# Performance work log

Measured on AMD Instinct MI355X. Metric: run time of the kernel, lower is better.

Reference implementation:

```python
import jax, jax.numpy as jnp
import numpy as np
from jax import lax

B, IMG, P, C_IN, E, H, NAX = 128, 224, 16, 1, 96, 4, 14
N = NAX * NAX  # 196 patches


def _ln(x, g, b, axes=(-1,)):
    mu = jnp.mean(x, axes, keepdims=True)
    v = jnp.var(x, axes, keepdims=True)
    return (x - mu) * lax.rsqrt(v + 1e-5) * g + b


def _embed3d(p):
    # p: [B, N, E]. Torch code rotates pair (2i,2i+1) by theta_i*col (row loop)
    # then theta_i*row (col loop) in-place => total angle theta_i*(row+col).
    bsz = p.shape[0]
    f = p.transpose(0, 2, 1).reshape(bsz, E, NAX, NAX)
    i = jnp.arange(E // 2, dtype=jnp.float32)
    theta = 10000.0 ** (-2.0 * i / E)  # [48]
    pos = jnp.arange(NAX, dtype=jnp.float32)
    ang = theta[:, None, None] * (pos[None, :, None] + pos[None, None, :])  # [48,14,14]
    cos, sin = jnp.cos(ang), jnp.sin(ang)
    xe, ye = f[:, 0::2], f[:, 1::2]  # [B,48,14,14] each
    rx = xe * cos - ye * sin
    ry = xe * sin + ye * cos
    f = jnp.stack([rx, ry], axis=2).reshape(bsz, E, NAX, NAX)  # re-interleave pairs
    return f.reshape(bsz, E, N).transpose(0, 2, 1)


def _mhsa(x, g, bt, Wqkv, bqkv, Wo, bo):
    # standard pre-norm residual MHSA block (MHSelfAttentionBlock assumed)
    h = _ln(x, g, bt)
    qkv = h @ Wqkv + bqkv  # [B,N,3E]
    q, k, v = jnp.split(qkv, 3, axis=-1)
    d = E // H
    def heads(t):
        return t.reshape(t.shape[0], N, H, d).transpose(0, 2, 1, 3)  # [B,H,N,d]
    q, k, v = heads(q), heads(k), heads(v)
    s = jnp.einsum('bhqd,bhkd->bhqk', q, k) / jnp.sqrt(jnp.float32(d))
    a = jax.nn.softmax(s, axis=-1)
    o = jnp.einsum('bhqk,bhkd->bhqd', a, v).transpose(0, 2, 1, 3).reshape(x.shape[0], N, E)
    return x + o @ Wo + bo


def _convT(x, w, b):
    # torch ConvTranspose2d(k=4, s=2, p=1); w: [C_in, C_out, 4, 4]
    wt = jnp.transpose(jnp.flip(w, (2, 3)), (1, 0, 2, 3))  # OIHW, flipped
    y = lax.conv_general_dilated(x, wt, (1, 1), ((2, 2), (2, 2)), lhs_dilation=(2, 2),
                                 dimension_numbers=('NCHW', 'OIHW', 'NCHW'))
    return y + b[None, :, None, None]


def _forward(x, timestep, Wp, bp, Wt1, bt1, Wt2, bt2,
             a0_g, a0_b, a0_Wqkv, a0_bqkv, a0_Wo, a0_bo,
             a1_g, a1_b, a1_Wqkv, a1_bqkv, a1_Wo, a1_bo,
             Wm0, bm0, Wm1, bm1, Wm2, bm2,
             Wd1, bd1, l1g, l1b, Wd2, bd2, l2g, l2b, Wd3, bd3, l3g, l3b, Wd4, bd4):
    # timestep embedding: emb = -log(0.5)*t -> [sin, cos] -> MLP
    e = 0.6931471805599453 * timestep[0]
    tv = jnp.stack([jnp.sin(e), jnp.cos(e)])  # [2]
    time = jax.nn.silu(tv @ Wt1 + bt1) @ Wt2 + bt2  # [E]
    # patch embed: conv stride 16
    p = lax.conv_general_dilated(x, Wp, (P, P), 'VALID',
                                 dimension_numbers=('NCHW', 'OIHW', 'NCHW'))
    p = (p + bp[None, :, None, None]).reshape(x.shape[0], E, N).transpose(0, 2, 1)  # [B,N,E]
    p = _embed3d(p)
    p = _mhsa(p, a0_g, a0_b, a0_Wqkv, a0_bqkv, a0_Wo, a0_bo)
    p = _mhsa(p, a1_g, a1_b, a1_Wqkv, a1_bqkv, a1_Wo, a1_bo)
    p = p + time
    p = jax.nn.silu(p @ Wm0 + bm0)
    p = jax.nn.silu(p @ Wm1 + bm1)
    p = jax.nn.silu(p @ Wm2 + bm2)
    # unpatchify decoder
    f = p.transpose(0, 2, 1).reshape(x.shape[0], E, NAX, NAX)
    f = jax.nn.silu(_ln(_convT(f, Wd1, bd1), l1g, l1b, (-2, -1)))  # [B,48,28,28]
    f = jax.nn.silu(_ln(_convT(f, Wd2, bd2), l2g, l2b, (-2, -1)))  # [B,24,56,56]
    f = jax.nn.silu(_ln(_convT(f, Wd3, bd3), l3g, l3b, (-2, -1)))  # [B,12,112,112]
    f = jax.nn.silu(_convT(f, Wd4, bd4))                            # [B,1,224,224]
    return jnp.clip(f, 0.0, 1.0)


def setup_inputs() -> dict:
    ks = jax.random.split(jax.random.key(0), 40)
    rn = lambda k, s: (jax.random.normal(k, s, jnp.float32) * 0.02)
    inp = {
        'x': jax.random.normal(ks[0], (B, C_IN, IMG, IMG), jnp.float32),
        'timestep': jax.random.uniform(ks[1], (1,), jnp.float32),
        'Wp': rn(ks[2], (E, C_IN, P, P)), 'bp': jnp.zeros((E,), jnp.float32),
        'Wt1': rn(ks[3], (2, 128)), 'bt1': jnp.zeros((128,), jnp.float32),
        'Wt2': rn(ks[4], (128, E)), 'bt2': jnp.zeros((E,), jnp.float32),
        'a0_g': jnp.ones((E,), jnp.float32), 'a0_b': jnp.zeros((E,), jnp.float32),
        'a0_Wqkv': rn(ks[5], (E, 3 * E)), 'a0_bqkv': jnp.zeros((3 * E,), jnp.float32),
        'a0_Wo': rn(ks[6], (E, E)), 'a0_bo': jnp.zeros((E,), jnp.float32),
        'a1_g': jnp.ones((E,), jnp.float32), 'a1_b': jnp.zeros((E,), jnp.float32),
        'a1_Wqkv': rn(ks[7], (E, 3 * E)), 'a1_bqkv': jnp.zeros((3 * E,), jnp.float32),
        'a1_Wo': rn(ks[8], (E, E)), 'a1_bo': jnp.zeros((E,), jnp.float32),
        'Wm0': rn(ks[9], (E, E)), 'bm0': jnp.zeros((E,), jnp.float32),
        'Wm1': rn(ks[10], (E, E)), 'bm1': jnp.zeros((E,), jnp.float32),
        'Wm2': rn(ks[11], (E, E)), 'bm2': jnp.zeros((E,), jnp.float32),
        'Wd1': rn(ks[12], (E, 48, 4, 4)), 'bd1': jnp.zeros((48,), jnp.float32),
        'l1g': jnp.ones((28, 28), jnp.float32), 'l1b': jnp.zeros((28, 28), jnp.float32),
        'Wd2': rn(ks[13], (48, 24, 4, 4)), 'bd2': jnp.zeros((24,), jnp.float32),
        'l2g': jnp.ones((56, 56), jnp.float32), 'l2b': jnp.zeros((56, 56), jnp.float32),
        'Wd3': rn(ks[14], (24, 12, 4, 4)), 'bd3': jnp.zeros((12,), jnp.float32),
        'l3g': jnp.ones((112, 112), jnp.float32), 'l3b': jnp.zeros((112, 112), jnp.float32),
        'Wd4': rn(ks[15], (12, 1, 4, 4)), 'bd4': jnp.zeros((1,), jnp.float32),
    }
    return inp


def reference(x, timestep, Wp, bp, Wt1, bt1, Wt2, bt2,
              a0_g, a0_b, a0_Wqkv, a0_bqkv, a0_Wo, a0_bo,
              a1_g, a1_b, a1_Wqkv, a1_bqkv, a1_Wo, a1_bo,
              Wm0, bm0, Wm1, bm1, Wm2, bm2,
              Wd1, bd1, l1g, l1b, Wd2, bd2, l2g, l2b, Wd3, bd3, l3g, l3b, Wd4, bd4):
    return _forward(x, timestep, Wp, bp, Wt1, bt1, Wt2, bt2,
                    a0_g, a0_b, a0_Wqkv, a0_bqkv, a0_Wo, a0_bo,
                    a1_g, a1_b, a1_Wqkv, a1_bqkv, a1_Wo, a1_bo,
                    Wm0, bm0, Wm1, bm1, Wm2, bm2,
                    Wd1, bd1, l1g, l1b, Wd2, bd2, l2g, l2b, Wd3, bd3, l3g, l3b, Wd4, bd4)
```

## Files before the change

kernel.cpp:

```cpp
#include <hip/hip_runtime.h>
#include <cmath>


#define B_   128
#define NPATCH 196
#define M_ROWS (B_*NPATCH)
#define E_   96

typedef _Float16 half8 __attribute__((ext_vector_type(8)));
typedef _Float16 half4v __attribute__((ext_vector_type(4)));
typedef float f32x4 __attribute__((ext_vector_type(4)));

__global__ void k_time(const float* __restrict__ ts,
                       const float* __restrict__ Wt1, const float* __restrict__ bt1,
                       const float* __restrict__ Wt2, const float* __restrict__ bt2,
                       float* __restrict__ timev)
{
    __shared__ float h[128];
    float e = 0.69314718055994530942f * ts[0];
    float sv = sinf(e), cv = cosf(e);
    int t = threadIdx.x;
    float z = sv * Wt1[t] + cv * Wt1[128 + t] + bt1[t];
    h[t] = z / (1.f + expf(-z));
    __syncthreads();
    if (t < 96) {
        float acc = bt2[t];
        for (int j = 0; j < 128; ++j) acc += h[j] * Wt2[j * 96 + t];
        timev[t] = acc;
    }
}

__global__ void __launch_bounds__(256) k_zstat(float* __restrict__ stat)
{
    int i = blockIdx.x * 256 + threadIdx.x;
    if (i < 21504) stat[i] = 0.f;
}

__global__ void __launch_bounds__(256) k_repack(const float* __restrict__ w1,
                                                const float* __restrict__ w2,
                                                const float* __restrict__ w3,
                                                const float* __restrict__ w4f,
                                                float* __restrict__ wr)
{
    int i = blockIdx.x * 256 + threadIdx.x;
    const float* src; int CIN, COUT, e; float* dst;
    if      (i < 73728) { src = w1;  CIN = 96; COUT = 48; e = i;          dst = wr; }
    else if (i < 92160) { src = w2;  CIN = 48; COUT = 24; e = i - 73728;  dst = wr + 73728; }
    else if (i < 96768) { src = w3;  CIN = 24; COUT = 12; e = i - 92160;  dst = wr + 92160; }
    else if (i < 96960) { src = w4f; CIN = 12; COUT = 1;  e = i - 96768;  dst = wr + 96768; }
    else return;
    int per = CIN * COUT * 4;
    int par = e / per, rem = e % per;
    int ci = rem / (COUT * 4);
    int o  = (rem >> 2) % COUT;
    int j  = rem & 3;
    int ry = par >> 1, rx = par & 1;
    int wy = (j < 2)  ? (3 - ry) : (1 - ry);
    int wx = (j & 1)  ? (1 - rx) : (3 - rx);
    dst[e] = src[(ci * COUT + o) * 16 + wy * 4 + wx];
}

__global__ void __launch_bounds__(256) k_wcvtc(const float* __restrict__ w1,
                                               _Float16* __restrict__ wc)
{
    int i = blockIdx.x * 256 + threadIdx.x;
    if (i >= 4 * 48 * 384) return;
    int p = i / 18432, rem = i % 18432;
    int o = rem / 384, k = rem % 384;
    int tap = k / 96, ci = k % 96;
    int ry = p >> 1, rx = p & 1;
    int wy = (tap < 2) ? (3 - ry) : (1 - ry);
    int wx = (tap & 1) ? (1 - rx) : (3 - rx);
    wc[i] = (_Float16)w1[(ci * 48 + o) * 16 + wy * 4 + wx];
}

__global__ void __launch_bounds__(256) k_wcvt2(const float* __restrict__ w2,
                                               _Float16* __restrict__ wc2)
{
    int i = blockIdx.x * 256 + threadIdx.x;
    if (i >= 4 * 32 * 192) return;
    int p = i / 6144, rem = i % 6144;
    int o = rem / 192, k = rem % 192;
    int tap = k / 48, ci = k % 48;
    int ry = p >> 1, rx = p & 1;
    int wy = (tap < 2) ? (3 - ry) : (1 - ry);
    int wx = (tap & 1) ? (1 - rx) : (3 - rx);
    wc2[i] = (o < 24) ? (_Float16)w2[(ci * 24 + o) * 16 + wy * 4 + wx]
                      : (_Float16)0.f;
}

__global__ void __launch_bounds__(256) k_wcvt3(const float* __restrict__ w3,
                                               _Float16* __restrict__ wc3)
{
    int i = blockIdx.x * 256 + threadIdx.x;
    if (i >= 4 * 16 * 96) return;
    int p = i / 1536, rem = i % 1536;
    int o = rem / 96, k = rem % 96;
    int tap = k / 24, ci = k % 24;
    int ry = p >> 1, rx = p & 1;
    int wy = (tap < 2) ? (3 - ry) : (1 - ry);
    int wx = (tap & 1) ? (1 - rx) : (3 - rx);
    wc3[i] = (o < 12) ? (_Float16)w3[(ci * 12 + o) * 16 + wy * 4 + wx]
                      : (_Float16)0.f;
}

__global__ void __launch_bounds__(256) k_wcvt(const float* __restrict__ qkv0,
                                              const float* __restrict__ qkv1,
                                              const float* __restrict__ wo0,
                                              const float* __restrict__ wo1,
                                              const float* __restrict__ wm0,
                                              const float* __restrict__ wm1,
                                              const float* __restrict__ wm2,
                                              _Float16* __restrict__ wh)
{
    int i = blockIdx.x * 256 + threadIdx.x;
    const float* src; int N; int e;
    if      (i < 27648)  { src = qkv0; N = 288; e = i; }
    else if (i < 55296)  { src = qkv1; N = 288; e = i - 27648; }
    else if (i < 64512)  { src = wo0;  N = 96;  e = i - 55296; }
    else if (i < 73728)  { src = wo1;  N = 96;  e = i - 64512; }
    else if (i < 82944)  { src = wm0;  N = 96;  e = i - 73728; }
    else if (i < 92160)  { src = wm1;  N = 96;  e = i - 82944; }
    else if (i < 101376) { src = wm2;  N = 96;  e = i - 92160; }
    else return;
    int n = e / 96, k = e % 96;
    wh[i] = (_Float16)src[k * N + n];
}

__global__ void __launch_bounds__(256) k_zb_h(_Float16* __restrict__ xinh)
{
    int i = blockIdx.x * 256 + threadIdx.x;
    if (i >= 128 * 60 * 96) return;
    int b = i / 5760, r = i % 5760;
    int pos = r / 96, ch = r % 96;
    int py, px;
    if      (pos < 16) { py = 0;        px = pos; }
    else if (pos < 32) { py = 15;       px = pos - 16; }
    else if (pos < 46) { py = pos - 31; px = 0; }
    else               { py = pos - 45; px = 15; }
    xinh[((size_t)(b * 256) + py * 16 + px) * 96 + ch] = (_Float16)0.f;
}

__global__ void __launch_bounds__(256) k_patch_mfma(const float* __restrict__ x,
                                                    const float* __restrict__ Wp,
                                                    const float* __restrict__ bp,
                                                    float* __restrict__ out)
{
    __shared__ __align__(16) _Float16 Ah[64 * 136];
    __shared__ __align__(16) _Float16 Wh[96 * 136];
    int t = threadIdx.x;
    int p0 = blockIdx.x * 64;
    int wave = t >> 6, lane = t & 63;
    int lm = lane & 15, quad = lane >> 4;
    f32x4 acc[6];
    #pragma unroll
    for (int nt = 0; nt < 6; ++nt) acc[nt] = (f32x4){0.f, 0.f, 0.f, 0.f};

    for (int kc = 0; kc < 2; ++kc) {
        __syncthreads();
        for (int i = t; i < 512; i += 256) {
            int lp = i >> 3, pyl = i & 7;
            int patch = p0 + lp;
            int b = patch / NPATCH, n = patch % NPATCH;
            int ny = n / 14, nx = n % 14;
            const float4* s4 = (const float4*)(x +
                ((size_t)(b * 224) + ny * 16 + kc * 8 + pyl) * 224 + nx * 16);
            float4 v0 = s4[0], v1 = s4[1], v2 = s4[2], v3 = s4[3];
            half8 h0, h1;
            h0[0]=(_Float16)v0.x; h0[1]=(_Float16)v0.y; h0[2]=(_Float16)v0.z; h0[3]=(_Float16)v0.w;
            h0[4]=(_Float16)v1.x; h0[5]=(_Float16)v1.y; h0[6]=(_Float16)v1.z; h0[7]=(_Float16)v1.w;
            h1[0]=(_Float16)v2.x; h1[1]=(_Float16)v2.y; h1[2]=(_Float16)v2.z; h1[3]=(_Float16)v2.w;
            h1[4]=(_Float16)v3.x; h1[5]=(_Float16)v3.y; h1[6]=(_Float16)v3.z; h1[7]=(_Float16)v3.w;
            *(half8*)&Ah[lp * 136 + pyl * 16]     = h0;
            *(half8*)&Ah[lp * 136 + pyl * 16 + 8] = h1;
        }
        for (int i = t; i < 1536; i += 256) {
            int e = i >> 4, s = i & 15;
            const float4* s4 = (const float4*)(Wp + e * 256 + kc * 128 + s * 8);
            float4 v0 = s4[0], v1 = s4[1];
            half8 h0;
            h0[0]=(_Float16)v0.x; h0[1]=(_Float16)v0.y; h0[2]=(_Float16)v0.z; h0[3]=(_Float16)v0.w;
            h0[4]=(_Float16)v1.x; h0[5]=(_Float16)v1.y; h0[6]=(_Float16)v1.z; h0[7]=(_Float16)v1.w;
            *(half8*)&Wh[e * 136 + s * 8] = h0;
        }
        __syncthreads();
        half8 af[4];
        #pragma unroll
        for (int ks = 0; ks < 4; ++ks)
            af[ks] = *(const half8*)&Ah[(wave * 16 + lm) * 136 + ks * 32 + quad * 8];
        #pragma unroll
        for (int ks = 0; ks < 4; ++ks) {
            #pragma unroll
            for (int nt = 0; nt < 6; ++nt) {
                half8 bf = *(const half8*)&Wh[(nt * 16 + lm) * 136 + ks * 32 + quad * 8];
                acc[nt] = __builtin_amdgcn_mfma_f32_16x16x32_f16(af[ks], bf, acc[nt], 0, 0, 0);
            }
        }
    }

    #pragma unroll
    for (int nt = 0; nt < 6; ++nt) {
        #pragma unroll
        for (int r = 0; r < 4; ++r) {
            int e = nt * 16 + lm;
            int lp = wave * 16 + quad * 4 + r;
            int patch = p0 + lp;
            int n = patch % NPATCH;
            int ny = n / 14, nx = n % 14;
            float yx = (float)(ny + nx);
            float v = acc[nt][r] + bp[e];
            float other = __shfl_xor(v, 1);
            float fi = (float)(e >> 1);
            float theta = expf(fi * (-2.f / 96.f) * 9.210340371976184f);
            float ang = theta * yx;
            float c = cosf(ang), s = sinf(ang);
            float outv = (lm & 1) ? (other * s + v * c) : (v * c - other * s);
            out[(size_t)patch * 96 + e] = outv;
        }
    }
}

__global__ void __launch_bounds__(256) k_ln_row(const float* __restrict__ x,
                                                const float* __restrict__ g,
                                                const float* __restrict__ bv,
                                                _Float16* __restrict__ out, int M)
{
    int lane = threadIdx.x & 63;
    int gw = (blockIdx.x * 256 + threadIdx.x) >> 6;
    int nw = (gridDim.x * 256) >> 6;
    float g0 = g[lane], b0 = bv[lane];
    float g1 = 0.f, b1 = 0.f;
    if (lane < 32) { g1 = g[64 + lane]; b1 = bv[64 + lane]; }
    for (int r = gw; r < M; r += nw) {
        const float* xr = x + (size_t)r * 96;
        float a = xr[lane];
        float c = (lane < 32) ? xr[64 + lane] : 0.f;
        float s = a + c, q = a * a + c * c;
        #pragma unroll
        for (int off = 32; off; off >>= 1) {
            s += __shfl_xor(s, off);
            q += __shfl_xor(q, off);
        }
        float mu = s * (1.f / 96.f);
        float rstd = rsqrtf(q * (1.f / 96.f) - mu * mu + 1e-5f);
        _Float16* orow = out + (size_t)r * 96;
        orow[lane] = (_Float16)((a - mu) * rstd * g0 + b0);
        if (lane < 32) orow[64 + lane] = (_Float16)((c - mu) * rstd * g1 + b1);
    }
}

template<int NCHUNKS, int OUTMODE, bool SILU, bool RES, bool ADDTIME, bool AHALF>
__global__ void __launch_bounds__(256) k_gemm_mfma(const void* __restrict__ A,
                                                   const _Float16* __restrict__ Wt,
                                                   const float* __restrict__ bias,
                                                   const float* __restrict__ res,
                                                   const float* __restrict__ timev,
                                                   void* __restrict__ outp)
{
    __shared__ __align__(16) _Float16 Ah[64 * 96];
    __shared__ __align__(16) _Float16 Wh[96 * 96];
    constexpr int NTOT = NCHUNKS * 96;
    int t = threadIdx.x;
    size_t row0 = (size_t)blockIdx.x * 64;

    if constexpr (AHALF) {
        const uint4* a4 = (const uint4*)((const _Float16*)A + row0 * 96);
        uint4* dst = (uint4*)Ah;
        for (int i = t; i < 768; i += 256) dst[i] = a4[i];
    } else {
        const float4* a4 = (const float4*)((const float*)A + row0 * 96);
        for (int i = t; i < 1536; i += 256) {
            float4 v = a4[i];
            half4v hv;
            hv[0] = (_Float16)v.x; hv[1] = (_Float16)v.y;
            hv[2] = (_Float16)v.z; hv[3] = (_Float16)v.w;
            *(half4v*)&Ah[i * 4] = hv;
        }
    }

    int wave = t >> 6, lane = t & 63;
    int lm = lane & 15, quad = lane >> 4;
    const f32x4 vzero = {0.f, 0.f, 0.f, 0.f};

    for (int ch = blockIdx.y; ch < NCHUNKS; ch += gridDim.y) {
        __syncthreads();
        {
            const uint4* src = (const uint4*)(Wt + (size_t)ch * 9216);
            uint4* dst = (uint4*)Wh;
            for (int i = t; i < 1152; i += 256) dst[i] = src[i];
        }
        __syncthreads();

        half8 af[3];
        #pragma unroll
        for (int ks = 0; ks < 3; ++ks)
            af[ks] = *(const half8*)&Ah[(wave * 16 + lm) * 96 + ks * 32 + quad * 8];

        f32x4 acc[6];
        #pragma unroll
        for (int ct = 0; ct < 6; ++ct) acc[ct] = vzero;

        #pragma unroll
        for (int ct = 0; ct < 6; ++ct) {
            #pragma unroll
            for (int ks = 0; ks < 3; ++ks) {
                half8 bf = *(const half8*)&Wh[(ct * 16 + lm) * 96 + ks * 32 + quad * 8];
                acc[ct] = __builtin_amdgcn_mfma_f32_16x16x32_f16(af[ks], bf, acc[ct], 0, 0, 0);
            }
        }

        #pragma unroll
        for (int ct = 0; ct < 6; ++ct) {
            #pragma unroll
            for (int r = 0; r < 4; ++r) {
                int lr = wave * 16 + quad * 4 + r;
                size_t row = row0 + lr;
                int lc = ct * 16 + lm;
                int col = ch * 96 + lc;
                float v = acc[ct][r] + bias[col];
                if constexpr (RES)     v += res[row * 96 + lc];
                if constexpr (ADDTIME) v += timev[lc];
                if constexpr (SILU)    v = v / (1.f + __expf(-v));
                if constexpr (OUTMODE == 0) {
                    ((float*)outp)[row * NTOT + col] = v;
                } else {
                    ((_Float16*)outp)[row * NTOT + col] = (_Float16)v;
                }
            }
        }
    }
}

__global__ void __launch_bounds__(256) k_mlp_fused(const _Float16* __restrict__ A,
                                                   const _Float16* __restrict__ W,
                                                   const float* __restrict__ b0,
                                                   const float* __restrict__ b1,
                                                   const float* __restrict__ b2,
                                                   _Float16* __restrict__ outh)
{
    __shared__ __align__(16) _Float16 Ah[2][64 * 96];
    __shared__ __align__(16) _Float16 Wh[3][96 * 96];
    int t = threadIdx.x;
    size_t row0 = (size_t)blockIdx.x * 64;

    {
        const uint4* a4 = (const uint4*)(A + row0 * 96);
        uint4* dst = (uint4*)&Ah[0][0];
        for (int i = t; i < 768; i += 256) dst[i] = a4[i];
    }
    {
        const uint4* src = (const uint4*)W;
        uint4* dst = (uint4*)&Wh[0][0];
        for (int i = t; i < 3456; i += 256) dst[i] = src[i];
    }

    int wave = t >> 6, lane = t & 63;
    int lm = lane & 15, quad = lane >> 4;
    const float* biases[3] = { b0, b1, b2 };
    int cur = 0;

    #pragma unroll
    for (int s = 0; s < 3; ++s) {
        __syncthreads();
        half8 af[3];
        #pragma unroll
        for (int ks = 0; ks < 3; ++ks)
            af[ks] = *(const half8*)&Ah[cur][(wave * 16 + lm) * 96 + ks * 32 + quad * 8];

        f32x4 acc[6];
        #pragma unroll
        for (int ct = 0; ct < 6; ++ct) acc[ct] = (f32x4){0.f, 0.f, 0.f, 0.f};

        #pragma unroll
        for (int ct = 0; ct < 6; ++ct) {
            #pragma unroll
            for (int ks = 0; ks < 3; ++ks) {
                half8 bf = *(const half8*)&Wh[s][(ct * 16 + lm) * 96 + ks * 32 + quad * 8];
                acc[ct] = __builtin_amdgcn_mfma_f32_16x16x32_f16(af[ks], bf, acc[ct], 0, 0, 0);
            }
        }

        const float* bias = biases[s];
        if (s < 2) {
            #pragma unroll
            for (int ct = 0; ct < 6; ++ct) {
                #pragma unroll
                for (int r = 0; r < 4; ++r) {
                    int lr = wave * 16 + quad * 4 + r;
                    int lc = ct * 16 + lm;
                    float v = acc[ct][r] + bias[lc];
                    v = v / (1.f + __expf(-v));
                    Ah[cur ^ 1][lr * 96 + lc] = (_Float16)v;
                }
            }
            cur ^= 1;
        } else {
            #pragma unroll
            for (int ct = 0; ct < 6; ++ct) {
                #pragma unroll
                for (int r = 0; r < 4; ++r) {
                    int lr = wave * 16 + quad * 4 + r;
                    size_t row = row0 + lr;
                    int lc = ct * 16 + lm;
                    float v = acc[ct][r] + bias[lc];
                    v = v / (1.f + __expf(-v));
                    size_t b = row / NPATCH; int n = (int)(row % NPATCH);
                    int ny = n / 14, nx = n % 14;
                    outh[((b * 256) + (1 + ny) * 16 + (1 + nx)) * 96 + lc] = (_Float16)v;
                }
            }
        }
    }
}

__global__ void __launch_bounds__(256) k_attn_mfma(const _Float16* __restrict__ qkv,
                                                   _Float16* __restrict__ o)
{
    __shared__ __align__(16) _Float16 Qs[208 * 40];
    __shared__ __align__(16) _Float16 Ks[208 * 40];
    __shared__ __align__(16) _Float16 Vt[32 * 232];
    __shared__ __align__(16) _Float16 Pw[4][16 * 232];

    int t = threadIdx.x;
    int bh = blockIdx.x;
    int b = bh >> 2, h = bh & 3;
    const _Float16* base = qkv + (size_t)b * NPATCH * 288 + h * 24;

    {
        const int4 z = {0, 0, 0, 0};
        int4* q4 = (int4*)Qs; int4* k4 = (int4*)Ks;
        for (int i = t; i < 1040; i += 256) { q4[i] = z; k4[i] = z; }
        int4* v4 = (int4*)Vt;
        for (int i = t; i < 928; i += 256) v4[i] = z;
        int4* p4 = (int4*)&Pw[0][0];
        for (int i = t; i < 1856; i += 256) p4[i] = z;
    }
    __syncthreads();

    for (int i = t; i < NPATCH * 24; i += 256) {
        int r = i / 24, d = i % 24;
        const _Float16* row = base + (size_t)r * 288;
        Qs[r * 40 + d]   = row[d];
        Ks[r * 40 + d]   = row[96 + d];
        Vt[d * 232 + r]  = row[192 + d];
    }
    __syncthreads();

    int wave = t >> 6, lane = t & 63;
    int lm = lane & 15, quad = lane >> 4;
    const float scale = 0.2041241452319315f;

    half8 bk[13];
    #pragma unroll
    for (int ct = 0; ct < 13; ++ct)
        bk[ct] = *(const half8*)&Ks[(ct * 16 + lm) * 40 + quad * 8];

    _Float16* pw = &Pw[wave][0];

    for (int rt = wave; rt < 13; rt += 4) {
        half8 aq = *(const half8*)&Qs[(rt * 16 + lm) * 40 + quad * 8];
        float rsum[4] = {0.f, 0.f, 0.f, 0.f};

        #pragma unroll
        for (int ct = 0; ct < 13; ++ct) {
            f32x4 s = (f32x4){0.f, 0.f, 0.f, 0.f};
            s = __builtin_amdgcn_mfma_f32_16x16x32_f16(aq, bk[ct], s, 0, 0, 0);
            #pragma unroll
            for (int r = 0; r < 4; ++r) {
                float p = __expf(fminf(s[r] * scale, 60.f));
                if (ct == 12 && lm >= 4) p = 0.f;
                rsum[r] += p;
                pw[(quad * 4 + r) * 232 + ct * 16 + lm] = (_Float16)p;
            }
        }

        #pragma unroll
        for (int r = 0; r < 4; ++r) {
            float s = rsum[r];
            s += __shfl_xor(s, 1);
            s += __shfl_xor(s, 2);
            s += __shfl_xor(s, 4);
            s += __shfl_xor(s, 8);
            rsum[r] = 1.f / s;
        }

        f32x4 ov0 = (f32x4){0.f, 0.f, 0.f, 0.f};
        f32x4 ov1 = (f32x4){0.f, 0.f, 0.f, 0.f};
        #pragma unroll
        for (int ks = 0; ks < 7; ++ks) {
            half8 ap = *(const half8*)&pw[lm * 232 + ks * 32 + quad * 8];
            half8 bv0 = *(const half8*)&Vt[(lm) * 232 + ks * 32 + quad * 8];
            half8 bv1 = *(const half8*)&Vt[(16 + lm) * 232 + ks * 32 + quad * 8];
            ov0 = __builtin_amdgcn_mfma_f32_16x16x32_f16(ap, bv0, ov0, 0, 0, 0);
            ov1 = __builtin_amdgcn_mfma_f32_16x16x32_f16(ap, bv1, ov1, 0, 0, 0);
        }

        #pragma unroll
        for (int r = 0; r < 4; ++r) {
            int row = rt * 16 + quad * 4 + r;
            if (row < NPATCH) {
                _Float16* orow = o + ((size_t)b * NPATCH + row) * 96 + h * 24;
                orow[lm] = (_Float16)(ov0[r] * rsum[r]);
                if (lm < 8) orow[16 + lm] = (_Float16)(ov1[r] * rsum[r]);
            }
        }
    }
}

__global__ void __launch_bounds__(256) k_conv1_tile(const _Float16* __restrict__ xinh,
                                                    const _Float16* __restrict__ wc,
                                                    const float* __restrict__ bias,
                                                    _Float16* __restrict__ c1,
                                                    float* __restrict__ pstat1)
{
    __shared__ __align__(16) _Float16 Xs[4 * 16 * 104];
    __shared__ float bins[96];
    int t = threadIdx.x;
    int blk = blockIdx.x;
    int b = blk / 7, s = blk % 7;

    if (t < 96) bins[t] = 0.f;

    for (int i = t; i < 768; i += 256) {
        int r = i / 192, rem = i % 192;
        int c = rem / 12, ch = (rem % 12) * 8;
        *(uint4*)&Xs[(r * 16 + c) * 104 + ch] =
            *(const uint4*)(xinh + ((size_t)(b * 256) + (2 * s + r) * 16 + c) * 96 + ch);
    }

    int wave = t >> 6, lane = t & 63;
    int lm = lane & 15, quad = lane >> 4;
    int ry = wave >> 1, rx = wave & 1;

    __syncthreads();

    for (int nt = 0; nt < 3; ++nt) {
        half8 bf[12];
        #pragma unroll
        for (int ks = 0; ks < 12; ++ks)
            bf[ks] = *(const half8*)&wc[((size_t)(wave * 48 + nt * 16 + lm)) * 384
                                        + ks * 32 + quad * 8];

        float sl = 0.f, ql = 0.f;
        #pragma unroll
        for (int rt = 0; rt < 2; ++rt) {
            int pp = rt * 16 + lm;
            int ppc = pp < 28 ? pp : 27;
            int pyl = ppc / 14, px = ppc % 14;

            half8 af[12];
            #pragma unroll
            for (int ks = 0; ks < 12; ++ks) {
                int k0 = ks * 32 + quad * 8;
                int tap = k0 / 96, off = k0 % 96;
                int dy = tap >> 1, dx = tap & 1;
                af[ks] = *(const half8*)&Xs[((pyl + ry + dy) * 16 + (px + rx + dx)) * 104 + off];
            }

            f32x4 acc = (f32x4){0.f, 0.f, 0.f, 0.f};
            #pragma unroll
            for (int ks = 0; ks < 12; ++ks)
                acc = __builtin_amdgcn_mfma_f32_16x16x32_f16(af[ks], bf[ks], acc, 0, 0, 0);

            #pragma unroll
            for (int r = 0; r < 4; ++r) {
                int pw = rt * 16 + quad * 4 + r;
                if (pw < 28) {
                    int pylw = pw / 14, pxw = pw % 14;
                    int oy = 2 * (2 * s + pylw) + ry, ox = 2 * pxw + rx;
                    float v = acc[r] + bias[nt * 16 + lm];
                    sl += v; ql += v * v;
                    c1[((size_t)(b * 28 + oy) * 28 + ox) * 48 + nt * 16 + lm] = (_Float16)v;
                }
            }
        }
        atomicAdd(&bins[(nt * 16 + lm) * 2],     sl);
        atomicAdd(&bins[(nt * 16 + lm) * 2 + 1], ql);
    }
    __syncthreads();
    if (t < 96) atomicAdd(&pstat1[(size_t)b * 96 + t], bins[t]);
}

__global__ void __launch_bounds__(256) k_ln1_apply(const _Float16* __restrict__ c1,
                                                   const float* __restrict__ pstat1,
                                                   const float* __restrict__ g,
                                                   const float* __restrict__ bv,
                                                   _Float16* __restrict__ xh)
{
    int i4 = blockIdx.x * 256 + threadIdx.x;
    int idx = i4 * 4;
    int ch = idx % 48;
    int t2 = idx / 48;
    int pos = t2 % 900;
    int b = t2 / 900;
    int py = pos / 30, px = pos % 30;
    half4v hv = (half4v){(_Float16)0.f, (_Float16)0.f, (_Float16)0.f, (_Float16)0.f};
    if (py >= 1 && py <= 28 && px >= 1 && px <= 28) {
        int j = (py - 1) * 28 + (px - 1);
        half4v v = *(const half4v*)&c1[((size_t)b * 784 + j) * 48 + ch];
        const float* ps = pstat1 + (size_t)b * 96 + ch * 2;
        float gj = g[j], bj = bv[j];
        #pragma unroll
        for (int k = 0; k < 4; ++k) {
            float mu = ps[2 * k] * (1.f / 784.f);
            float rstd = rsqrtf(ps[2 * k + 1] * (1.f / 784.f) - mu * mu + 1e-5f);
            float u = ((float)v[k] - mu) * rstd * gj + bj;
            hv[k] = (_Float16)(u / (1.f + __expf(-u)));
        }
    }
    *(half4v*)&xh[idx] = hv;
}

__global__ void __launch_bounds__(256) k_conv2_tile(const _Float16* __restrict__ xh,
                                                    const _Float16* __restrict__ wc,
                                                    const float* __restrict__ bias,
                                                    _Float16* __restrict__ c2,
                                                    float* __restrict__ pstat2)
{
    __shared__ __align__(16) _Float16 Xs[4 * 30 * 56];
    __shared__ float bins[48];
    int t = threadIdx.x;
    int blk = blockIdx.x;
    int b = blk / 14, s = blk % 14;

    if (t < 48) bins[t] = 0.f;

    for (int i = t; i < 720; i += 256) {
        int r = i / 180, rem = i % 180;
        int c = rem / 6, ch = (rem % 6) * 8;
        *(uint4*)&Xs[(r * 30 + c) * 56 + ch] =
            *(const uint4*)(xh + ((size_t)(b * 900) + (2 * s + r) * 30 + c) * 48 + ch);
    }

    int wave = t >> 6, lane = t & 63;
    int lm = lane & 15, quad = lane >> 4;
    int ry = wave >> 1, rx = wave & 1;

    half8 bf0[6], bf1[6];
    #pragma unroll
    for (int ks = 0; ks < 6; ++ks) {
        bf0[ks] = *(const half8*)&wc[((size_t)(wave * 32 + lm)) * 192 + ks * 32 + quad * 8];
        bf1[ks] = *(const half8*)&wc[((size_t)(wave * 32 + 16 + lm)) * 192 + ks * 32 + quad * 8];
    }

    __syncthreads();

    float s0l = 0.f, q0l = 0.f, s1l = 0.f, q1l = 0.f;
    #pragma unroll
    for (int rt = 0; rt < 4; ++rt) {
        int pp = rt * 16 + lm;
        int ppc = pp < 56 ? pp : 55;
        int pyl = ppc / 28, px = ppc % 28;

        half8 af[6];
        #pragma unroll
        for (int ks = 0; ks < 6; ++ks) {
            int k0 = ks * 32 + quad * 8;
            int tap = k0 / 48, off = k0 % 48;
            int dy = tap >> 1, dx = tap & 1;
            af[ks] = *(const half8*)&Xs[((pyl + ry + dy) * 30 + (px + rx + dx)) * 56 + off];
        }

        f32x4 acc0 = (f32x4){0.f, 0.f, 0.f, 0.f};
        f32x4 acc1 = (f32x4){0.f, 0.f, 0.f, 0.f};
        #pragma unroll
        for (int ks = 0; ks < 6; ++ks) {
            acc0 = __builtin_amdgcn_mfma_f32_16x16x32_f16(af[ks], bf0[ks], acc0, 0, 0, 0);
            acc1 = __builtin_amdgcn_mfma_f32_16x16x32_f16(af[ks], bf1[ks], acc1, 0, 0, 0);
        }

        #pragma unroll
        for (int r = 0; r < 4; ++r) {
            int pw = rt * 16 + quad * 4 + r;
            if (pw < 56) {
                int pylw = pw / 28, pxw = pw % 28;
                int oy = 2 * (2 * s + pylw) + ry, ox = 2 * pxw + rx;
                _Float16* orow = c2 + ((size_t)(b * 56 + oy) * 56 + ox) * 24;
                float v0 = acc0[r] + bias[lm];
                orow[lm] = (_Float16)v0;
                s0l += v0; q0l += v0 * v0;
                if (lm < 8) {
                    float v1 = acc1[r] + bias[16 + lm];
                    orow[16 + lm] = (_Float16)v1;
                    s1l += v1; q1l += v1 * v1;
                }
            }
        }
    }
    atomicAdd(&bins[lm * 2],     s0l);
    atomicAdd(&bins[lm * 2 + 1], q0l);
    if (lm < 8) {
        atomicAdd(&bins[(16 + lm) * 2],     s1l);
        atomicAdd(&bins[(16 + lm) * 2 + 1], q1l);
    }
    __syncthreads();
    if (t < 48) atomicAdd(&pstat2[(size_t)b * 48 + t], bins[t]);
}

__global__ void __launch_bounds__(256) k_ln2_apply(const _Float16* __restrict__ c2,
                                                   const float* __restrict__ pstat2,
                                                   const float* __restrict__ g,
                                                   const float* __restrict__ bv,
                                                   _Float16* __restrict__ xh)
{
    int i4 = blockIdx.x * 256 + threadIdx.x;
    int idx = i4 * 4;
    int ch = idx % 24;
    int t2 = idx / 24;
    int pos = t2 % 3364;
    int b = t2 / 3364;
    int py = pos / 58, px = pos % 58;
    half4v hv = (half4v){(_Float16)0.f, (_Float16)0.f, (_Float16)0.f, (_Float16)0.f};
    if (py >= 1 && py <= 56 && px >= 1 && px <= 56) {
        int j = (py - 1) * 56 + (px - 1);
        half4v v = *(const half4v*)&c2[((size_t)b * 3136 + j) * 24 + ch];
        const float* ps = pstat2 + (size_t)b * 48 + ch * 2;
        float gj = g[j], bj = bv[j];
        #pragma unroll
        for (int k = 0; k < 4; ++k) {
            float mu = ps[2 * k] * (1.f / 3136.f);
            float rstd = rsqrtf(ps[2 * k + 1] * (1.f / 3136.f) - mu * mu + 1e-5f);
            float u = ((float)v[k] - mu) * rstd * gj + bj;
            hv[k] = (_Float16)(u / (1.f + __expf(-u)));
        }
    }
    *(half4v*)&xh[idx] = hv;
}

__global__ void __launch_bounds__(256) k_conv3_tile(const _Float16* __restrict__ xh,
                                                    const _Float16* __restrict__ wc,
                                                    const float* __restrict__ bias,
                                                    _Float16* __restrict__ c3,
                                                    float* __restrict__ pstat3)
{
    __shared__ __align__(16) _Float16 Xs[3 * 58 * 40];
    __shared__ float bins[24];
    int t = threadIdx.x;
    int blk = blockIdx.x;
    int b = blk / 56, s = blk % 56;

    if (t < 24) bins[t] = 0.f;

    for (int i = t; i < 522; i += 256) {
        int r = i / 174, rem = i % 174;
        int c = rem / 3, ch = (rem % 3) * 8;
        *(uint4*)&Xs[(r * 58 + c) * 40 + ch] =
            *(const uint4*)(xh + ((size_t)(b * 3364) + (s + r) * 58 + c) * 24 + ch);
    }

    int wave = t >> 6, lane = t & 63;
    int lm = lane & 15, quad = lane >> 4;
    int ry = wave >> 1, rx = wave & 1;

    half8 bf[3];
    #pragma unroll
    for (int ks = 0; ks < 3; ++ks)
        bf[ks] = *(const half8*)&wc[((size_t)(wave * 16 + lm)) * 96 + ks * 32 + quad * 8];

    __syncthreads();

    float sl = 0.f, ql = 0.f;
    #pragma unroll
    for (int rt = 0; rt < 4; ++rt) {
        int px = rt * 16 + lm;
        int pxc = px < 56 ? px : 55;

        half8 af[3];
        #pragma unroll
        for (int ks = 0; ks < 3; ++ks) {
            int k0 = ks * 32 + quad * 8;
            int tap = k0 / 24, off = k0 % 24;
            int dy = tap >> 1, dx = tap & 1;
            af[ks] = *(const half8*)&Xs[((ry + dy) * 58 + (pxc + rx + dx)) * 40 + off];
        }

        f32x4 acc = (f32x4){0.f, 0.f, 0.f, 0.f};
        #pragma unroll
        for (int ks = 0; ks < 3; ++ks)
            acc = __builtin_amdgcn_mfma_f32_16x16x32_f16(af[ks], bf[ks], acc, 0, 0, 0);

        if (lm < 12) {
            #pragma unroll
            for (int r = 0; r < 4; ++r) {
                int pw = rt * 16 + quad * 4 + r;
                if (pw < 56) {
                    int oy = 2 * s + ry, ox = 2 * pw + rx;
                    float v = acc[r] + bias[lm];
                    sl += v; ql += v * v;
                    c3[((size_t)(b * 112 + oy) * 112 + ox) * 12 + lm] = (_Float16)v;
                }
            }
        }
    }
    if (lm < 12) {
        atomicAdd(&bins[lm * 2],     sl);
        atomicAdd(&bins[lm * 2 + 1], ql);
    }
    __syncthreads();
    if (t < 24) atomicAdd(&pstat3[(size_t)b * 24 + t], bins[t]);
}

__global__ void __launch_bounds__(256) k_ln3_apply(const _Float16* __restrict__ c3,
                                                   const float* __restrict__ pstat3,
                                                   const float* __restrict__ g,
                                                   const float* __restrict__ bv,
                                                   _Float16* __restrict__ xh4)
{
    int i4 = blockIdx.x * 256 + threadIdx.x;
    int idx = i4 * 4;
    int ch = idx % 12;
    int t2 = idx / 12;
    int pix = t2 % 12544;
    int b = t2 / 12544;
    half4v v = *(const half4v*)&c3[idx];
    const float* ps = pstat3 + (size_t)b * 24 + ch * 2;
    float gp = g[pix], bp = bv[pix];
    half4v hv;
    #pragma unroll
    for (int k = 0; k < 4; ++k) {
        float mu = ps[2 * k] * (1.f / 12544.f);
        float rstd = rsqrtf(ps[2 * k + 1] * (1.f / 12544.f) - mu * mu + 1e-5f);
        float u = ((float)v[k] - mu) * rstd * gp + bp;
        hv[k] = (_Float16)(u / (1.f + __expf(-u)));
    }
    *(half4v*)&xh4[idx] = hv;
}

__global__ void __launch_bounds__(256) k_conv_final2(const _Float16* __restrict__ x,
                                                     const float* __restrict__ wr,
                                                     const float* __restrict__ bias,
                                                     float* __restrict__ out)
{
    constexpr int HIN = 112, CIN = 12;
    int rem = blockIdx.x * 256 + threadIdx.x;
    int b   = rem / (HIN * HIN);
    int pix = rem % (HIN * HIN);
    int py = pix / HIN, px = pix % HIN;
    const _Float16* xb = x + (size_t)b * (HIN * HIN * CIN);
    const float4* w4 = (const float4*)wr;

    float acc00 = 0.f, acc01 = 0.f, acc10 = 0.f, acc11 = 0.f;

    #pragma unroll
    for (int a = 0; a < 3; ++a) {
        int row = py - 1 + a;
        bool rv = (a == 1) || (row >= 0 && row < HIN);
        #pragma unroll
        for (int c = 0; c < 3; ++c) {
            int col = px - 1 + c;
            bool cv = (c == 1) || (col >= 0 && col < HIN);
            float tv[12];
            if (rv && cv) {
                const _Float16* p = xb + ((size_t)(row * HIN + col)) * CIN;
                half4v h0 = *(const half4v*)&p[0];
                half4v h1 = *(const half4v*)&p[4];
                half4v h2 = *(const half4v*)&p[8];
                #pragma unroll
                for (int j = 0; j < 4; ++j) {
                    tv[j]     = (float)h0[j];
                    tv[4 + j] = (float)h1[j];
                    tv[8 + j] = (float)h2[j];
                }
            } else {
                #pragma unroll
                for (int j = 0; j < 12; ++j) tv[j] = 0.f;
            }
            #pragma unroll
            for (int ry = 0; ry < 2; ++ry) {
                int dy = a - ry;
                if (dy < 0 || dy > 1) continue;
                #pragma unroll
                for (int rx = 0; rx < 2; ++rx) {
                    int dx = c - rx;
                    if (dx < 0 || dx > 1) continue;
                    int j = dy * 2 + dx;
                    const float4* wp = w4 + (ry * 2 + rx) * 12;
                    float sacc = 0.f;
                    #pragma unroll
                    for (int ci = 0; ci < 12; ++ci) {
                        float4 W = wp[ci];
                        float wj = (j == 0) ? W.x : (j == 1) ? W.y : (j == 2) ? W.z : W.w;
                        sacc += tv[ci] * wj;
                    }
                    if (ry == 0) { if (rx == 0) acc00 += sacc; else acc01 += sacc; }
                    else         { if (rx == 0) acc10 += sacc; else acc11 += sacc; }
                }
            }
        }
    }

    float bb = bias[0];
    float u00 = acc00 + bb, u01 = acc01 + bb, u10 = acc10 + bb, u11 = acc11 + bb;
    u00 = u00 / (1.f + __expf(-u00));
    u01 = u01 / (1.f + __expf(-u01));
    u10 = u10 / (1.f + __expf(-u10));
    u11 = u11 / (1.f + __expf(-u11));
    float2 v0, v1;
    v0.x = fminf(fmaxf(u00, 0.f), 1.f);
    v0.y = fminf(fmaxf(u01, 0.f), 1.f);
    v1.x = fminf(fmaxf(u10, 0.f), 1.f);
    v1.y = fminf(fmaxf(u11, 0.f), 1.f);
    float* ob = out + (size_t)b * 50176;
    *(float2*)(ob + (2 * py) * 224 + 2 * px)     = v0;
    *(float2*)(ob + (2 * py + 1) * 224 + 2 * px) = v1;
}

extern "C" void kernel_launch(void* const* d_in, const int* in_sizes, int n_in,
                              void* d_out, int out_size, void* d_ws, size_t ws_size,
                              hipStream_t stream)
{
    const float* x       = (const float*)d_in[0];
    const float* ts      = (const float*)d_in[1];
    const float* Wp      = (const float*)d_in[2];
    const float* bp      = (const float*)d_in[3];
    const float* Wt1     = (const float*)d_in[4];
    const float* bt1     = (const float*)d_in[5];
    const float* Wt2     = (const float*)d_in[6];
    const float* bt2     = (const float*)d_in[7];
    const float* a0_g    = (const float*)d_in[8];
    const float* a0_b    = (const float*)d_in[9];
    const float* a0_Wqkv = (const float*)d_in[10];
    const float* a0_bqkv = (const float*)d_in[11];
    const float* a0_Wo   = (const float*)d_in[12];
    const float* a0_bo   = (const float*)d_in[13];
    const float* a1_g    = (const float*)d_in[14];
    const float* a1_b    = (const float*)d_in[15];
    const float* a1_Wqkv = (const float*)d_in[16];
    const float* a1_bqkv = (const float*)d_in[17];
    const float* a1_Wo   = (const float*)d_in[18];
    const float* a1_bo   = (const float*)d_in[19];
    const float* Wm0     = (const float*)d_in[20];
    const float* bm0     = (const float*)d_in[21];
    const float* Wm1     = (const float*)d_in[22];
    const float* bm1     = (const float*)d_in[23];
    const float* Wm2     = (const float*)d_in[24];
    const float* bm2     = (const float*)d_in[25];
    const float* Wd1     = (const float*)d_in[26];
    const float* bd1     = (const float*)d_in[27];
    const float* l1g     = (const float*)d_in[28];
    const float* l1b     = (const float*)d_in[29];
    const float* Wd2     = (const float*)d_in[30];
    const float* bd2     = (const float*)d_in[31];
    const float* l2g     = (const float*)d_in[32];
    const float* l2b     = (const float*)d_in[33];
    const float* Wd3     = (const float*)d_in[34];
    const float* bd3     = (const float*)d_in[35];
    const float* l3g     = (const float*)d_in[36];
    const float* l3b     = (const float*)d_in[37];
    const float* Wd4     = (const float*)d_in[38];
    const float* bd4     = (const float*)d_in[39];
    float* out = (float*)d_out;

    const size_t R = 2408448;
    float* ws   = (float*)d_ws;
    float* tvec = ws;
    float* p0   = ws + 512;
    _Float16* p0h  = (_Float16*)(ws + 512);
    _Float16* hh   = (_Float16*)(ws + 512 + R);
    _Float16* qkvh = (_Float16*)(ws + 512 + 2 * R);
    _Float16* obh  = (_Float16*)(ws + 512 + 5 * R);
    float* p1   = ws + 512 + 6 * R;
    _Float16* xinh = (_Float16*)(ws + 512 + 2 * R);
    _Float16* C1h  = (_Float16*)(ws + 512 + 5 * R);
    _Float16* xh2  = (_Float16*)(ws + 512 + 7 * R);
    _Float16* C2h  = (_Float16*)(ws + 512);
    _Float16* xh3  = (_Float16*)(ws + 512 + 7 * R + 5529600);
    _Float16* C3h  = (_Float16*)(ws + 512);
    _Float16* xh4  = (_Float16*)(ws + 512 + 7 * R + 5529600);
    float* Wr   = ws + 512 + 7 * R + 5529600 + 10334208;
    _Float16* WH = (_Float16*)(Wr + 96960);
    _Float16* Wc  = (_Float16*)Wr;
    _Float16* Wc2 = (_Float16*)(Wr + 36864);
    _Float16* Wc3 = (_Float16*)(Wr + 49152);
    float* stat = Wr + 96960 + 50688;
    float* stat1 = stat;
    float* stat2 = stat + 12288;
    float* stat3 = stat + 18432;
    const size_t NEED = (512 + 7 * R + 5529600 + 10334208 + 96960 + 50688 + 21504 + 16)
                        * sizeof(float);
    if (ws_size < NEED) return;

    _Float16* WHqkv0 = WH;
    _Float16* WHqkv1 = WH + 27648;
    _Float16* WHwo0  = WH + 55296;
    _Float16* WHwo1  = WH + 64512;
    _Float16* WHwm0  = WH + 73728;

    k_time<<<1, 128, 0, stream>>>(ts, Wt1, bt1, Wt2, bt2, tvec);
    k_zstat<<<84, 256, 0, stream>>>(stat);
    k_repack<<<379, 256, 0, stream>>>(Wd1, Wd2, Wd3, Wd4, Wr);
    k_wcvtc<<<288, 256, 0, stream>>>(Wd1, Wc);
    k_wcvt2<<<96, 256, 0, stream>>>(Wd2, Wc2);
    k_wcvt3<<<24, 256, 0, stream>>>(Wd3, Wc3);
    k_wcvt<<<396, 256, 0, stream>>>(a0_Wqkv, a1_Wqkv, a0_Wo, a1_Wo,
                                    Wm0, Wm1, Wm2, WH);
    k_patch_mfma<<<M_ROWS / 64, 256, 0, stream>>>(x, Wp, bp, p0);

    k_ln_row<<<1024, 256, 0, stream>>>(p0, a0_g, a0_b, hh, M_ROWS);
    k_gemm_mfma<3, 1, false, false, false, true><<<dim3(M_ROWS / 64, 3), 256, 0, stream>>>(
        hh, WHqkv0, a0_bqkv, nullptr, nullptr, qkvh);
    k_attn_mfma<<<B_ * 4, 256, 0, stream>>>(qkvh, obh);
    k_gemm_mfma<1, 0, false, true, false, true><<<dim3(M_ROWS / 64, 1), 256, 0, stream>>>(
        obh, WHwo0, a0_bo, p0, nullptr, p1);

    k_ln_row<<<1024, 256, 0, stream>>>(p1, a1_g, a1_b, hh, M_ROWS);
    k_gemm_mfma<3, 1, false, false, false, true><<<dim3(M_ROWS / 64, 3), 256, 0, stream>>>(
        hh, WHqkv1, a1_bqkv, nullptr, nullptr, qkvh);
    k_attn_mfma<<<B_ * 4, 256, 0, stream>>>(qkvh, obh);
    k_gemm_mfma<1, 1, false, true, true, true><<<dim3(M_ROWS / 64, 1), 256, 0, stream>>>(
        obh, WHwo1, a1_bo, p1, tvec, p0h);

    k_zb_h<<<2880, 256, 0, stream>>>(xinh);

    k_mlp_fused<<<M_ROWS / 64, 256, 0, stream>>>(p0h, WHwm0, bm0, bm1, bm2, xinh);

    k_conv1_tile<<<B_ * 7, 256, 0, stream>>>(xinh, Wc, bd1, C1h, stat1);
    k_ln1_apply<<<5400, 256, 0, stream>>>(C1h, stat1, l1g, l1b, xh2);
    k_conv2_tile<<<B_ * 14, 256, 0, stream>>>(xh2, Wc2, bd2, C2h, stat2);
    k_ln2_apply<<<10092, 256, 0, stream>>>(C2h, stat2, l2g, l2b, xh3);
    k_conv3_tile<<<B_ * 56, 256, 0, stream>>>(xh3, Wc3, bd3, C3h, stat3);
    k_ln3_apply<<<18816, 256, 0, stream>>>(C3h, stat3, l3g, l3b, xh4);
    k_conv_final2<<<6272, 256, 0, stream>>>(xh4, Wr + 96768, bd4, out);
}
```

Before: 464.7 us.

## Tile final transposed conv through LDS and use fp16 dot2 accumulation

```diff
diff --git a/kernel.cpp b/kernel.cpp
--- a/kernel.cpp
+++ b/kernel.cpp
@@ -9,6 +9,7 @@
 
 typedef _Float16 half8 __attribute__((ext_vector_type(8)));
 typedef _Float16 half4v __attribute__((ext_vector_type(4)));
+typedef _Float16 half2v __attribute__((ext_vector_type(2)));
 typedef float f32x4 __attribute__((ext_vector_type(4)));
 
 __global__ void k_time(const float* __restrict__ ts,
@@ -58,6 +59,16 @@
     int wy = (j < 2)  ? (3 - ry) : (1 - ry);
     int wx = (j & 1)  ? (1 - rx) : (3 - rx);
     dst[e] = src[(ci * COUT + o) * 16 + wy * 4 + wx];
+}
+
+__global__ void k_wcvt4(const float* __restrict__ wr4,
+                        _Float16* __restrict__ wcf)
+{
+    int i = threadIdx.x;
+    if (i >= 192) return;
+    int p = i / 48, rem = i % 48;
+    int j = rem / 12, ci = rem % 12;
+    wcf[(p * 4 + j) * 12 + ci] = (_Float16)wr4[p * 48 + ci * 4 + j];
 }
 
 __global__ void __launch_bounds__(256) k_wcvtc(const float* __restrict__ w1,
@@ -826,83 +837,91 @@
     *(half4v*)&xh4[idx] = hv;
 }
 
-__global__ void __launch_bounds__(256) k_conv_final2(const _Float16* __restrict__ x,
-                                                     const float* __restrict__ wr,
+__global__ void __launch_bounds__(256) k_conv_final3(const _Float16* __restrict__ x,
+                                                     const _Float16* __restrict__ wcf,
                                                      const float* __restrict__ bias,
                                                      float* __restrict__ out)
 {
     constexpr int HIN = 112, CIN = 12;
-    int rem = blockIdx.x * 256 + threadIdx.x;
-    int b   = rem / (HIN * HIN);
-    int pix = rem % (HIN * HIN);
-    int py = pix / HIN, px = pix % HIN;
-    const _Float16* xb = x + (size_t)b * (HIN * HIN * CIN);
-    const float4* w4 = (const float4*)wr;
-
-    float acc00 = 0.f, acc01 = 0.f, acc10 = 0.f, acc11 = 0.f;
-
+    __shared__ __align__(16) _Float16 Xs[4 * 114 * 12];
+    __shared__ __align__(16) _Float16 Wl[192];
+    int t = threadIdx.x;
+    int blk = blockIdx.x;
+    int b = blk / 56, s = blk % 56;
+    int py0 = 2 * s;
+
+    {
+        const int4 z = {0, 0, 0, 0};
+        int4* p4 = (int4*)Xs;
+        for (int i = t; i < 684; i += 256) p4[i] = z;
+        if (t < 24) *(int4*)&Wl[t * 8] = *(const int4*)&wcf[t * 8];
+    }
+    __syncthreads();
+    for (int i = t; i < 672; i += 256) {
+        int r = i / 168, rem = i % 168;
+        int row = py0 - 1 + r;
+        if (row >= 0 && row < HIN) {
+            *(uint4*)&Xs[(size_t)r * 1368 + rem * 8] =
+                *(const uint4*)(x + ((size_t)b * HIN * HIN + (size_t)row * HIN) * CIN + rem * 8);
+        }
+    }
+    __syncthreads();
+
+    if (t >= 224) return;
+    int pyl = t / 112;
+    int px = t % 112;
+    int py = py0 + pyl;
+
+    half2v tvp[9][6];
     #pragma unroll
     for (int a = 0; a < 3; ++a) {
-        int row = py - 1 + a;
-        bool rv = (a == 1) || (row >= 0 && row < HIN);
+        int lr = pyl + a;
         #pragma unroll
         for (int c = 0; c < 3; ++c) {
             int col = px - 1 + c;
-            bool cv = (c == 1) || (col >= 0 && col < HIN);
-            float tv[12];
-            if (rv && cv) {
-                const _Float16* p = xb + ((size_t)(row * HIN + col)) * CIN;
-                half4v h0 = *(const half4v*)&p[0];
-                half4v h1 = *(const half4v*)&p[4];
-                half4v h2 = *(const half4v*)&p[8];
+            int cs = (col < 0) ? 113 : col;
+            const _Float16* p = &Xs[((size_t)lr * 114 + cs) * 12];
+            half4v h0 = *(const half4v*)&p[0];
+            half4v h1 = *(const half4v*)&p[4];
+            half4v h2 = *(const half4v*)&p[8];
+            int ti = a * 3 + c;
+            tvp[ti][0] = (half2v){h0[0], h0[1]};
+            tvp[ti][1] = (half2v){h0[2], h0[3]};
+            tvp[ti][2] = (half2v){h1[0], h1[1]};
+            tvp[ti][3] = (half2v){h1[2], h1[3]};
+            tvp[ti][4] = (half2v){h2[0], h2[1]};
+            tvp[ti][5] = (half2v){h2[2], h2[3]};
+        }
+    }
+
+    float bb = bias[0];
+    float* ob = out + (size_t)b * 50176;
+    #pragma unroll
+    for (int ry = 0; ry < 2; ++ry) {
+        float res[2];
+        #pragma unroll
+        for (int rx = 0; rx < 2; ++rx) {
+            int p = ry * 2 + rx;
+            float acc = 0.f;
+            #pragma unroll
+            for (int dy = 0; dy < 2; ++dy) {
                 #pragma unroll
-                for (int j = 0; j < 4; ++j) {
-                    tv[j]     = (float)h0[j];
-                    tv[4 + j] = (float)h1[j];
-                    tv[8 + j] = (float)h2[j];
+                for (int dx = 0; dx < 2; ++dx) {
+                    int j = dy * 2 + dx;
+                    int ti = (ry + dy) * 3 + (rx + dx);
+                    const half2v* wp = (const half2v*)&Wl[(p * 4 + j) * 12];
+                    #pragma unroll
+                    for (int k = 0; k < 6; ++k)
+                        acc = __builtin_amdgcn_fdot2(tvp[ti][k], wp[k], acc, false);
                 }
-            } else {
-                #pragma unroll
-                for (int j = 0; j < 12; ++j) tv[j] = 0.f;
-            }
-            #pragma unroll
-            for (int ry = 0; ry < 2; ++ry) {
-                int dy = a - ry;
-                if (dy < 0 || dy > 1) continue;
-                #pragma unroll
-                for (int rx = 0; rx < 2; ++rx) {
-                    int dx = c - rx;
-                    if (dx < 0 || dx > 1) continue;
-                    int j = dy * 2 + dx;
-                    const float4* wp = w4 + (ry * 2 + rx) * 12;
-                    float sacc = 0.f;
-                    #pragma unroll
-                    for (int ci = 0; ci < 12; ++ci) {
-                        float4 W = wp[ci];
-                        float wj = (j == 0) ? W.x : (j == 1) ? W.y : (j == 2) ? W.z : W.w;
-                        sacc += tv[ci] * wj;
-                    }
-                    if (ry == 0) { if (rx == 0) acc00 += sacc; else acc01 += sacc; }
-                    else         { if (rx == 0) acc10 += sacc; else acc11 += sacc; }
-                }
-            }
-        }
-    }
-
-    float bb = bias[0];
-    float u00 = acc00 + bb, u01 = acc01 + bb, u10 = acc10 + bb, u11 = acc11 + bb;
-    u00 = u00 / (1.f + __expf(-u00));
-    u01 = u01 / (1.f + __expf(-u01));
-    u10 = u10 / (1.f + __expf(-u10));
-    u11 = u11 / (1.f + __expf(-u11));
-    float2 v0, v1;
-    v0.x = fminf(fmaxf(u00, 0.f), 1.f);
-    v0.y = fminf(fmaxf(u01, 0.f), 1.f);
-    v1.x = fminf(fmaxf(u10, 0.f), 1.f);
-    v1.y = fminf(fmaxf(u11, 0.f), 1.f);
-    float* ob = out + (size_t)b * 50176;
-    *(float2*)(ob + (2 * py) * 224 + 2 * px)     = v0;
-    *(float2*)(ob + (2 * py + 1) * 224 + 2 * px) = v1;
+            }
+            float u = acc + bb;
+            u = u / (1.f + __expf(-u));
+            res[rx] = fminf(fmaxf(u, 0.f), 1.f);
+        }
+        float2 v; v.x = res[0]; v.y = res[1];
+        *(float2*)(ob + (size_t)(2 * py + ry) * 224 + 2 * px) = v;
+    }
 }
 
 extern "C" void kernel_launch(void* const* d_in, const int* in_sizes, int n_in,
@@ -976,7 +995,8 @@
     float* stat1 = stat;
     float* stat2 = stat + 12288;
     float* stat3 = stat + 18432;
-    const size_t NEED = (512 + 7 * R + 5529600 + 10334208 + 96960 + 50688 + 21504 + 16)
+    _Float16* Wcf = (_Float16*)(stat + 21504);
+    const size_t NEED = (512 + 7 * R + 5529600 + 10334208 + 96960 + 50688 + 21504 + 128)
                         * sizeof(float);
     if (ws_size < NEED) return;
 
@@ -989,6 +1009,7 @@
     k_time<<<1, 128, 0, stream>>>(ts, Wt1, bt1, Wt2, bt2, tvec);
     k_zstat<<<84, 256, 0, stream>>>(stat);
     k_repack<<<379, 256, 0, stream>>>(Wd1, Wd2, Wd3, Wd4, Wr);
+    k_wcvt4<<<1, 192, 0, stream>>>(Wr + 96768, Wcf);
     k_wcvtc<<<288, 256, 0, stream>>>(Wd1, Wc);
     k_wcvt2<<<96, 256, 0, stream>>>(Wd2, Wc2);
     k_wcvt3<<<24, 256, 0, stream>>>(Wd3, Wc3);
@@ -1020,5 +1041,5 @@
     k_ln2_apply<<<10092, 256, 0, stream>>>(C2h, stat2, l2g, l2b, xh3);
     k_conv3_tile<<<B_ * 56, 256, 0, stream>>>(xh3, Wc3, bd3, C3h, stat3);
     k_ln3_apply<<<18816, 256, 0, stream>>>(C3h, stat3, l3g, l3b, xh4);
-    k_conv_final2<<<6272, 256, 0, stream>>>(xh4, Wr + 96768, bd4, out);
-}
+    k_conv_final3<<<7168, 256, 0, stream>>>(xh4, Wcf, bd4, out);
+}
```

New measurement: 483.1 us. 1.04x slower.
